# Performance work log

Hardware: AMD Instinct MI355X
Metric: run time of the kernel (lower is better)

The kernel has to match this reference:

```python
import jax, jax.numpy as jnp
import numpy as np

S, B, E, D, A = 4096, 16, 1024, 1024, 512


def setup_inputs() -> dict:
    key = jax.random.key(0)
    ks = jax.random.split(key, 8)
    inv = lambda n: 1.0 / np.sqrt(n)
    return {
        "encoder_padded_last_layer_states": jax.random.normal(ks[0], (S, B, E), jnp.float32),
        "decoder_previous_time_step_state": jax.random.normal(ks[1], (1, B, D), jnp.float32),
        "We": jax.random.uniform(ks[2], (E, A), jnp.float32, -inv(E), inv(E)),
        "be": jax.random.uniform(ks[3], (A,), jnp.float32, -inv(E), inv(E)),
        "Wd": jax.random.uniform(ks[4], (D, A), jnp.float32, -inv(D), inv(D)),
        "bd": jax.random.uniform(ks[5], (A,), jnp.float32, -inv(D), inv(D)),
        "Ws": jax.random.uniform(ks[6], (A, 1), jnp.float32, -inv(A), inv(A)),
        "bs": jax.random.uniform(ks[7], (1,), jnp.float32, -inv(A), inv(A)),
    }


def reference(encoder_padded_last_layer_states, decoder_previous_time_step_state,
              We, be, Wd, bd, Ws, bs):
    enc = encoder_padded_last_layer_states  # [S, B, E]
    dec = decoder_previous_time_step_state  # [1, B, D]
    weighted_e = enc @ We + be              # [S, B, A]
    weighted_d = dec @ Wd + bd              # [1, B, A] broadcasts over S
    scores = jnp.tanh(weighted_e + weighted_d) @ Ws + bs  # [S, B, 1]
    alpha = jax.nn.softmax(scores, axis=0)  # softmax over time dim
    # alpha^T [B,1,S] bmm enc^T [B,S,E] -> [B,1,E] -> squeeze -> [B,E]
    contexts = jnp.einsum("sbo,sbe->be", alpha, enc)
    return contexts
```

## Files before the change

### kernel.cpp

```cpp
#include <hip/hip_runtime.h>
#include <hip/hip_bf16.h>

#define S_DIM 4096
#define B_DIM 16
#define E_DIM 1024
#define D_DIM 1024
#define A_DIM 512
#define M_DIM (S_DIM * B_DIM)

typedef __bf16 bf16x8 __attribute__((ext_vector_type(8)));
typedef float f32x4 __attribute__((ext_vector_type(4)));
typedef unsigned short u16;

__device__ __forceinline__ u16 f2bf(float f) {
    unsigned u = __builtin_bit_cast(unsigned, f);
    u += 0x7fffu + ((u >> 16) & 1u);
    return (u16)(u >> 16);
}

__global__ void k_transpose_we(const float* __restrict__ We, u16* __restrict__ WeT) {
    __shared__ float tile[32][33];
    const int e0 = blockIdx.x * 32;
    const int a0 = blockIdx.y * 32;
    const int tx = threadIdx.x, ty = threadIdx.y;
#pragma unroll
    for (int i = 0; i < 32; i += 8)
        tile[ty + i][tx] = We[(size_t)(e0 + ty + i) * A_DIM + a0 + tx];
    __syncthreads();
#pragma unroll
    for (int i = 0; i < 32; i += 8)
        WeT[(size_t)(a0 + ty + i) * E_DIM + e0 + tx] = f2bf(tile[tx][ty + i]);
}

__global__ void k_comb(const float* __restrict__ dec, const float* __restrict__ Wd,
                       const float* __restrict__ bd, const float* __restrict__ be,
                       float* __restrict__ comb) {
    const int a = blockIdx.x * 256 + threadIdx.x;
    const int b = blockIdx.y;
    float acc = bd[a] + be[a];
    const float* dptr = dec + (size_t)b * D_DIM;
    for (int d = 0; d < D_DIM; ++d)
        acc += dptr[d] * Wd[(size_t)d * A_DIM + a];
    comb[b * A_DIM + a] = acc;
}

__global__ __launch_bounds__(512, 4)
void k_scores(const float* __restrict__ enc, const u16* __restrict__ WeT,
              const float* __restrict__ comb, const float* __restrict__ Wsv,
              const float* __restrict__ bs, float* __restrict__ scores) {
    __shared__ u16 As[64 * 40];
    __shared__ u16 Bs[512 * 40];
    __shared__ float sred[64];

    const int tid  = threadIdx.x;
    const int lane = tid & 63;
    const int wave = tid >> 6;
    const int wr = wave >> 2;
    const int wc = wave & 3;
    const int l15 = lane & 15, lhi = lane >> 4;
    const int blockRow = blockIdx.x * 64;

    if (tid < 64) sred[tid] = 0.f;

    f32x4 acc[2][8];
#pragma unroll
    for (int mf = 0; mf < 2; ++mf)
#pragma unroll
        for (int nf = 0; nf < 8; ++nf)
            acc[mf][nf] = f32x4{0.f, 0.f, 0.f, 0.f};

    const int arow = tid >> 3, ach = tid & 7;
    const int brow = tid >> 2, bch = tid & 3;

    for (int k0 = 0; k0 < E_DIM; k0 += 32) {
        {
            const float4 v = *reinterpret_cast<const float4*>(
                enc + (size_t)(blockRow + arow) * E_DIM + k0 + ach * 4);
            ushort4 h;
            h.x = f2bf(v.x); h.y = f2bf(v.y); h.z = f2bf(v.z); h.w = f2bf(v.w);
            *reinterpret_cast<ushort4*>(&As[arow * 40 + ach * 4]) = h;
        }
#pragma unroll
        for (int p = 0; p < 4; ++p) {
            const int a = brow + p * 128;
            const uint4 w = *reinterpret_cast<const uint4*>(
                WeT + (size_t)a * E_DIM + k0 + bch * 8);
            *reinterpret_cast<uint4*>(&Bs[a * 40 + bch * 8]) = w;
        }
        __syncthreads();

        bf16x8 af[2];
#pragma unroll
        for (int mf = 0; mf < 2; ++mf)
            af[mf] = *reinterpret_cast<const bf16x8*>(
                &As[(wr * 32 + mf * 16 + l15) * 40 + lhi * 8]);
#pragma unroll
        for (int nf = 0; nf < 8; ++nf) {
            const bf16x8 bfv = *reinterpret_cast<const bf16x8*>(
                &Bs[(wc * 128 + nf * 16 + l15) * 40 + lhi * 8]);
            acc[0][nf] = __builtin_amdgcn_mfma_f32_16x16x32_bf16(af[0], bfv, acc[0][nf], 0, 0, 0);
            acc[1][nf] = __builtin_amdgcn_mfma_f32_16x16x32_bf16(af[1], bfv, acc[1][nf], 0, 0, 0);
        }
        __syncthreads();
    }

    float part[2][4] = {{0, 0, 0, 0}, {0, 0, 0, 0}};
#pragma unroll
    for (int nf = 0; nf < 8; ++nf) {
        const int C = wc * 128 + nf * 16 + l15;
        const float wsv = Wsv[C];
#pragma unroll
        for (int mf = 0; mf < 2; ++mf) {
#pragma unroll
            for (int j = 0; j < 4; ++j) {
                const int Rl = wr * 32 + mf * 16 + lhi * 4 + j;
                const int b = (blockRow + Rl) & (B_DIM - 1);
                const float x = acc[mf][nf][j] + comb[b * A_DIM + C];
                const float e = __expf(-2.f * fabsf(x));
                float th = (1.f - e) / (1.f + e);
                th = (x < 0.f) ? -th : th;
                part[mf][j] += th * wsv;
            }
        }
    }
#pragma unroll
    for (int off = 1; off < 16; off <<= 1)
#pragma unroll
        for (int mf = 0; mf < 2; ++mf)
#pragma unroll
            for (int j = 0; j < 4; ++j)
                part[mf][j] += __shfl_xor(part[mf][j], off, 64);
    if (l15 == 0) {
#pragma unroll
        for (int mf = 0; mf < 2; ++mf)
#pragma unroll
            for (int j = 0; j < 4; ++j)
                atomicAdd(&sred[wr * 32 + mf * 16 + lhi * 4 + j], part[mf][j]);
    }
    __syncthreads();
    if (tid < 64) {
        const int r = blockRow + tid;
        scores[(size_t)(r & (B_DIM - 1)) * S_DIM + (r >> 4)] = sred[tid] + bs[0];
    }
}

__global__ void k_softmax(const float* __restrict__ scores, float* __restrict__ alpha) {
    __shared__ float red[8];
    const int b = blockIdx.x;
    const int tid = threadIdx.x;
    const float* sc = scores + (size_t)b * S_DIM;
    float m = -1e30f;
    for (int i = tid; i < S_DIM; i += 256) m = fmaxf(m, sc[i]);
#pragma unroll
    for (int off = 32; off; off >>= 1) m = fmaxf(m, __shfl_xor(m, off, 64));
    if ((tid & 63) == 0) red[tid >> 6] = m;
    __syncthreads();
    m = fmaxf(fmaxf(red[0], red[1]), fmaxf(red[2], red[3]));
    float s = 0.f;
    for (int i = tid; i < S_DIM; i += 256) s += __expf(sc[i] - m);
#pragma unroll
    for (int off = 32; off; off >>= 1) s += __shfl_xor(s, off, 64);
    if ((tid & 63) == 0) red[4 + (tid >> 6)] = s;
    __syncthreads();
    const float inv = 1.f / (red[4] + red[5] + red[6] + red[7]);
    float* al = alpha + (size_t)b * S_DIM;
    for (int i = tid; i < S_DIM; i += 256) al[i] = __expf(sc[i] - m) * inv;
}

__global__ void k_context(const float* __restrict__ enc, const float* __restrict__ alpha,
                          float* __restrict__ out) {
    const int b = blockIdx.y;
    const int chunk = blockIdx.x;
    const int tid = threadIdx.x;
    const int s0 = chunk * 64;
    float4 accv = make_float4(0.f, 0.f, 0.f, 0.f);
    for (int s = 0; s < 64; ++s) {
        const float al = alpha[(size_t)b * S_DIM + s0 + s];
        const float4 v = *reinterpret_cast<const float4*>(
            enc + ((size_t)(s0 + s) * B_DIM + b) * E_DIM + tid * 4);
        accv.x += al * v.x; accv.y += al * v.y;
        accv.z += al * v.z; accv.w += al * v.w;
    }
    float* o = out + (size_t)b * E_DIM + tid * 4;
    atomicAdd(o + 0, accv.x);
    atomicAdd(o + 1, accv.y);
    atomicAdd(o + 2, accv.z);
    atomicAdd(o + 3, accv.w);
}

extern "C" void kernel_launch(void* const* d_in, const int* in_sizes, int n_in,
                              void* d_out, int out_size, void* d_ws, size_t ws_size,
                              hipStream_t stream) {
    const float* enc = (const float*)d_in[0];
    const float* dec = (const float*)d_in[1];
    const float* We  = (const float*)d_in[2];
    const float* be  = (const float*)d_in[3];
    const float* Wd  = (const float*)d_in[4];
    const float* bd  = (const float*)d_in[5];
    const float* Ws  = (const float*)d_in[6];
    const float* bs  = (const float*)d_in[7];
    float* out = (float*)d_out;

    char* ws = (char*)d_ws;
    u16*   WeT    = (u16*)ws;
    float* comb   = (float*)(ws + (1 << 20));
    float* scores = (float*)(ws + (1 << 20) + (32 << 10));
    float* alpha  = (float*)(ws + (1 << 20) + (32 << 10) + (256 << 10));

    hipLaunchKernelGGL(k_transpose_we, dim3(E_DIM / 32, A_DIM / 32), dim3(32, 8), 0, stream,
                       We, WeT);
    hipLaunchKernelGGL(k_comb, dim3(A_DIM / 256, B_DIM), dim3(256), 0, stream,
                       dec, Wd, bd, be, comb);
    hipLaunchKernelGGL(k_scores, dim3(M_DIM / 64), dim3(512), 0, stream,
                       enc, WeT, comb, Ws, bs, scores);
    hipLaunchKernelGGL(k_softmax, dim3(B_DIM), dim3(256), 0, stream, scores, alpha);
    hipMemsetAsync(d_out, 0, (size_t)B_DIM * E_DIM * sizeof(float), stream);
    hipLaunchKernelGGL(k_context, dim3(S_DIM / 64, B_DIM), dim3(256), 0, stream,
                       enc, alpha, out);
}
```

Baseline: 543.6 us.

## Rework score GEMM with swizzled pre-tiled weights, direct LDS loads, and deterministic context reduction

Weights are pre-converted to bf16 in per-K-slab tiles with an XOR swizzle, so the score GEMM can stream them straight into LDS via global_load_lds. The GEMM block drops to 256 threads with 4x8 MFMA tiles per wave and K slabs of 64, and the combined bias is cached in LDS for the tanh epilogue. The decoder projection is split across four waves and reduced in shared memory. The bs bias is dropped because softmax ignores a constant shift. The context atomics and memset are replaced by a two-pass partial-sum reduction. The risks are lower occupancy and larger LDS use per block.

New measurement: 490.5 us. 1.11x faster.

```diff
diff --git a/kernel.cpp b/kernel.cpp
--- a/kernel.cpp
+++ b/kernel.cpp
@@ -7,6 +7,9 @@
 #define D_DIM 1024
 #define A_DIM 512
 #define M_DIM (S_DIM * B_DIM)
+#define BK 64
+#define NKS (E_DIM / BK)
+#define MT 64
 
 typedef __bf16 bf16x8 __attribute__((ext_vector_type(8)));
 typedef float f32x4 __attribute__((ext_vector_type(4)));
@@ -17,105 +20,139 @@
     u += 0x7fffu + ((u >> 16) & 1u);
     return (u16)(u >> 16);
 }
-
-__global__ void k_transpose_we(const float* __restrict__ We, u16* __restrict__ WeT) {
-    __shared__ float tile[32][33];
-    const int e0 = blockIdx.x * 32;
-    const int a0 = blockIdx.y * 32;
-    const int tx = threadIdx.x, ty = threadIdx.y;
-#pragma unroll
-    for (int i = 0; i < 32; i += 8)
-        tile[ty + i][tx] = We[(size_t)(e0 + ty + i) * A_DIM + a0 + tx];
-    __syncthreads();
-#pragma unroll
-    for (int i = 0; i < 32; i += 8)
-        WeT[(size_t)(a0 + ty + i) * E_DIM + e0 + tx] = f2bf(tile[tx][ty + i]);
+__device__ __forceinline__ unsigned pack2(float a, float b) {
+    return (unsigned)f2bf(a) | ((unsigned)f2bf(b) << 16);
+}
+
+__device__ __forceinline__ void gload_lds16(const void* g, void* l) {
+    __builtin_amdgcn_global_load_lds(
+        (const __attribute__((address_space(1))) unsigned*)g,
+        (__attribute__((address_space(3))) unsigned*)l, 16, 0, 0);
+}
+
+__global__ void k_prep_we(const float* __restrict__ We, u16* __restrict__ WeT) {
+    const int gid = blockIdx.x * 256 + threadIdx.x;
+    const int ks = gid >> 12, rem = gid & 4095;
+    const int a = rem >> 3, d = rem & 7;
+    const int c = d ^ (a & 7);
+    const int e0 = ks * BK + c * 8;
+    float v[8];
+#pragma unroll
+    for (int i = 0; i < 8; ++i) v[i] = We[(size_t)(e0 + i) * A_DIM + a];
+    uint4 h;
+    h.x = pack2(v[0], v[1]); h.y = pack2(v[2], v[3]);
+    h.z = pack2(v[4], v[5]); h.w = pack2(v[6], v[7]);
+    *reinterpret_cast<uint4*>(WeT + (size_t)ks * A_DIM * BK + a * BK + d * 8) = h;
 }
 
 __global__ void k_comb(const float* __restrict__ dec, const float* __restrict__ Wd,
                        const float* __restrict__ bd, const float* __restrict__ be,
                        float* __restrict__ comb) {
-    const int a = blockIdx.x * 256 + threadIdx.x;
+    __shared__ float red[4][64];
+    const int a0 = blockIdx.x * 64;
     const int b = blockIdx.y;
-    float acc = bd[a] + be[a];
-    const float* dptr = dec + (size_t)b * D_DIM;
-    for (int d = 0; d < D_DIM; ++d)
-        acc += dptr[d] * Wd[(size_t)d * A_DIM + a];
-    comb[b * A_DIM + a] = acc;
-}
-
-__global__ __launch_bounds__(512, 4)
+    const int t = threadIdx.x;
+    const int al = t & 63, w = t >> 6;
+    float acc = 0.f;
+    const float* dp = dec + (size_t)b * D_DIM + w * 256;
+    const float* wp = Wd + (size_t)w * 256 * A_DIM + a0 + al;
+    for (int d = 0; d < 256; ++d)
+        acc += dp[d] * wp[(size_t)d * A_DIM];
+    red[w][al] = acc;
+    __syncthreads();
+    if (t < 64)
+        comb[b * A_DIM + a0 + t] =
+            red[0][t] + red[1][t] + red[2][t] + red[3][t] + bd[a0 + t] + be[a0 + t];
+}
+
+__global__ __launch_bounds__(256, 2)
 void k_scores(const float* __restrict__ enc, const u16* __restrict__ WeT,
               const float* __restrict__ comb, const float* __restrict__ Wsv,
-              const float* __restrict__ bs, float* __restrict__ scores) {
-    __shared__ u16 As[64 * 40];
-    __shared__ u16 Bs[512 * 40];
-    __shared__ float sred[64];
-
-    const int tid  = threadIdx.x;
+              float* __restrict__ scores) {
+    __shared__ __align__(16) u16 As[MT * BK];
+    __shared__ __align__(16) u16 Bs[A_DIM * BK];
+
+    const int tid = threadIdx.x;
     const int lane = tid & 63;
-    const int wave = tid >> 6;
-    const int wr = wave >> 2;
-    const int wc = wave & 3;
+    const int wc = tid >> 6;
     const int l15 = lane & 15, lhi = lane >> 4;
-    const int blockRow = blockIdx.x * 64;
-
-    if (tid < 64) sred[tid] = 0.f;
-
-    f32x4 acc[2][8];
-#pragma unroll
-    for (int mf = 0; mf < 2; ++mf)
+    const int blockRow = blockIdx.x * MT;
+
+    f32x4 acc[4][8];
+#pragma unroll
+    for (int mf = 0; mf < 4; ++mf)
 #pragma unroll
         for (int nf = 0; nf < 8; ++nf)
             acc[mf][nf] = f32x4{0.f, 0.f, 0.f, 0.f};
 
-    const int arow = tid >> 3, ach = tid & 7;
-    const int brow = tid >> 2, bch = tid & 3;
-
-    for (int k0 = 0; k0 < E_DIM; k0 += 32) {
-        {
-            const float4 v = *reinterpret_cast<const float4*>(
-                enc + (size_t)(blockRow + arow) * E_DIM + k0 + ach * 4);
-            ushort4 h;
-            h.x = f2bf(v.x); h.y = f2bf(v.y); h.z = f2bf(v.z); h.w = f2bf(v.w);
-            *reinterpret_cast<ushort4*>(&As[arow * 40 + ach * 4]) = h;
-        }
-#pragma unroll
-        for (int p = 0; p < 4; ++p) {
-            const int a = brow + p * 128;
-            const uint4 w = *reinterpret_cast<const uint4*>(
-                WeT + (size_t)a * E_DIM + k0 + bch * 8);
-            *reinterpret_cast<uint4*>(&Bs[a * 40 + bch * 8]) = w;
+    const int bOff = wc * 16384 + lane * 16;
+
+    for (int ks = 0; ks < NKS; ++ks) {
+        const int k0 = ks * BK;
+        const char* gsrc = (const char*)WeT + (size_t)ks * A_DIM * BK * 2 + bOff;
+        char* ldst = (char*)Bs + bOff;
+#pragma unroll
+        for (int i = 0; i < 16; ++i)
+            gload_lds16(gsrc + i * 1024, ldst + i * 1024);
+#pragma unroll
+        for (int h = 0; h < 2; ++h) {
+            const int g = tid + h * 256;
+            const int r = g >> 3, d = g & 7;
+            const int c = d ^ (r & 7);
+            const float* src = enc + (size_t)(blockRow + r) * E_DIM + k0 + c * 8;
+            const float4 v0 = *reinterpret_cast<const float4*>(src);
+            const float4 v1 = *reinterpret_cast<const float4*>(src + 4);
+            uint4 hh;
+            hh.x = pack2(v0.x, v0.y); hh.y = pack2(v0.z, v0.w);
+            hh.z = pack2(v1.x, v1.y); hh.w = pack2(v1.z, v1.w);
+            *reinterpret_cast<uint4*>((char*)As + r * 128 + d * 16) = hh;
         }
         __syncthreads();
-
-        bf16x8 af[2];
-#pragma unroll
-        for (int mf = 0; mf < 2; ++mf)
-            af[mf] = *reinterpret_cast<const bf16x8*>(
-                &As[(wr * 32 + mf * 16 + l15) * 40 + lhi * 8]);
-#pragma unroll
-        for (int nf = 0; nf < 8; ++nf) {
-            const bf16x8 bfv = *reinterpret_cast<const bf16x8*>(
-                &Bs[(wc * 128 + nf * 16 + l15) * 40 + lhi * 8]);
-            acc[0][nf] = __builtin_amdgcn_mfma_f32_16x16x32_bf16(af[0], bfv, acc[0][nf], 0, 0, 0);
-            acc[1][nf] = __builtin_amdgcn_mfma_f32_16x16x32_bf16(af[1], bfv, acc[1][nf], 0, 0, 0);
+#pragma unroll
+        for (int kk = 0; kk < 2; ++kk) {
+            bf16x8 af[4];
+#pragma unroll
+            for (int mf = 0; mf < 4; ++mf) {
+                const int rr = mf * 16 + l15;
+                af[mf] = *reinterpret_cast<const bf16x8*>(
+                    (const char*)As + rr * 128 + ((kk * 64 + lhi * 16) ^ ((rr & 7) << 4)));
+            }
+#pragma unroll
+            for (int nf = 0; nf < 8; ++nf) {
+                const int br = wc * 128 + nf * 16 + l15;
+                const bf16x8 bfv = *reinterpret_cast<const bf16x8*>(
+                    (const char*)Bs + br * 128 + ((kk * 64 + lhi * 16) ^ ((br & 7) << 4)));
+#pragma unroll
+                for (int mf = 0; mf < 4; ++mf)
+                    acc[mf][nf] = __builtin_amdgcn_mfma_f32_16x16x32_bf16(
+                        af[mf], bfv, acc[mf][nf], 0, 0, 0);
+            }
         }
         __syncthreads();
     }
 
-    float part[2][4] = {{0, 0, 0, 0}, {0, 0, 0, 0}};
+    float* combLDS = reinterpret_cast<float*>(Bs);
+    float* sred = reinterpret_cast<float*>(As);
+#pragma unroll
+    for (int i = 0; i < 8; ++i) {
+        const int idx = tid + i * 256;
+        reinterpret_cast<float4*>(combLDS)[idx] = reinterpret_cast<const float4*>(comb)[idx];
+    }
+    if (tid < MT) sred[tid] = 0.f;
+    __syncthreads();
+
+    float part[4][4] = {};
 #pragma unroll
     for (int nf = 0; nf < 8; ++nf) {
         const int C = wc * 128 + nf * 16 + l15;
         const float wsv = Wsv[C];
 #pragma unroll
-        for (int mf = 0; mf < 2; ++mf) {
+        for (int mf = 0; mf < 4; ++mf) {
 #pragma unroll
             for (int j = 0; j < 4; ++j) {
-                const int Rl = wr * 32 + mf * 16 + lhi * 4 + j;
+                const int Rl = mf * 16 + lhi * 4 + j;
                 const int b = (blockRow + Rl) & (B_DIM - 1);
-                const float x = acc[mf][nf][j] + comb[b * A_DIM + C];
+                const float x = acc[mf][nf][j] + combLDS[b * A_DIM + C];
                 const float e = __expf(-2.f * fabsf(x));
                 float th = (1.f - e) / (1.f + e);
                 th = (x < 0.f) ? -th : th;
@@ -126,21 +163,21 @@
 #pragma unroll
     for (int off = 1; off < 16; off <<= 1)
 #pragma unroll
-        for (int mf = 0; mf < 2; ++mf)
+        for (int mf = 0; mf < 4; ++mf)
 #pragma unroll
             for (int j = 0; j < 4; ++j)
                 part[mf][j] += __shfl_xor(part[mf][j], off, 64);
     if (l15 == 0) {
 #pragma unroll
-        for (int mf = 0; mf < 2; ++mf)
+        for (int mf = 0; mf < 4; ++mf)
 #pragma unroll
             for (int j = 0; j < 4; ++j)
-                atomicAdd(&sred[wr * 32 + mf * 16 + lhi * 4 + j], part[mf][j]);
-    }
-    __syncthreads();
-    if (tid < 64) {
-        const int r = blockRow + tid;
-        scores[(size_t)(r & (B_DIM - 1)) * S_DIM + (r >> 4)] = sred[tid] + bs[0];
+                atomicAdd(&sred[mf * 16 + lhi * 4 + j], part[mf][j]);
+    }
+    __syncthreads();
+    if (tid < MT) {
+        const int rr = blockRow + tid;
+        scores[(size_t)(rr & (B_DIM - 1)) * S_DIM + (rr >> 4)] = sred[tid];
     }
 }
 
@@ -167,25 +204,29 @@
     for (int i = tid; i < S_DIM; i += 256) al[i] = __expf(sc[i] - m) * inv;
 }
 
-__global__ void k_context(const float* __restrict__ enc, const float* __restrict__ alpha,
-                          float* __restrict__ out) {
-    const int b = blockIdx.y;
-    const int chunk = blockIdx.x;
-    const int tid = threadIdx.x;
-    const int s0 = chunk * 64;
-    float4 accv = make_float4(0.f, 0.f, 0.f, 0.f);
+__global__ void k_ctx1(const float* __restrict__ enc, const float* __restrict__ alpha,
+                       float* __restrict__ partial) {
+    const int b = blockIdx.y, ch = blockIdx.x, tid = threadIdx.x;
+    const int s0 = ch * 64;
+    float4 av = make_float4(0.f, 0.f, 0.f, 0.f);
+    const float* al = alpha + (size_t)b * S_DIM + s0;
     for (int s = 0; s < 64; ++s) {
-        const float al = alpha[(size_t)b * S_DIM + s0 + s];
+        const float a = al[s];
         const float4 v = *reinterpret_cast<const float4*>(
             enc + ((size_t)(s0 + s) * B_DIM + b) * E_DIM + tid * 4);
-        accv.x += al * v.x; accv.y += al * v.y;
-        accv.z += al * v.z; accv.w += al * v.w;
-    }
-    float* o = out + (size_t)b * E_DIM + tid * 4;
-    atomicAdd(o + 0, accv.x);
-    atomicAdd(o + 1, accv.y);
-    atomicAdd(o + 2, accv.z);
-    atomicAdd(o + 3, accv.w);
+        av.x += a * v.x; av.y += a * v.y; av.z += a * v.z; av.w += a * v.w;
+    }
+    reinterpret_cast<float4*>(partial)[((size_t)b * 64 + ch) * 256 + tid] = av;
+}
+
+__global__ void k_ctx2(const float* __restrict__ partial, float* __restrict__ out) {
+    const int b = blockIdx.x, tid = threadIdx.x;
+    float4 s = make_float4(0.f, 0.f, 0.f, 0.f);
+    for (int c = 0; c < 64; ++c) {
+        const float4 v = reinterpret_cast<const float4*>(partial)[((size_t)b * 64 + c) * 256 + tid];
+        s.x += v.x; s.y += v.y; s.z += v.z; s.w += v.w;
+    }
+    reinterpret_cast<float4*>(out)[b * 256 + tid] = s;
 }
 
 extern "C" void kernel_launch(void* const* d_in, const int* in_sizes, int n_in,
@@ -198,23 +239,22 @@
     const float* Wd  = (const float*)d_in[4];
     const float* bd  = (const float*)d_in[5];
     const float* Ws  = (const float*)d_in[6];
-    const float* bs  = (const float*)d_in[7];
     float* out = (float*)d_out;
 
     char* ws = (char*)d_ws;
-    u16*   WeT    = (u16*)ws;
-    float* comb   = (float*)(ws + (1 << 20));
-    float* scores = (float*)(ws + (1 << 20) + (32 << 10));
-    float* alpha  = (float*)(ws + (1 << 20) + (32 << 10) + (256 << 10));
-
-    hipLaunchKernelGGL(k_transpose_we, dim3(E_DIM / 32, A_DIM / 32), dim3(32, 8), 0, stream,
-                       We, WeT);
-    hipLaunchKernelGGL(k_comb, dim3(A_DIM / 256, B_DIM), dim3(256), 0, stream,
+    u16*   WeT     = (u16*)ws;
+    float* comb    = (float*)(ws + (1 << 20));
+    float* scores  = (float*)(ws + (1 << 20) + (32 << 10));
+    float* alpha   = (float*)(ws + (1 << 20) + (288 << 10));
+    float* partial = (float*)(ws + (1 << 20) + (544 << 10));
+
+    hipLaunchKernelGGL(k_prep_we, dim3(256), dim3(256), 0, stream, We, WeT);
+    hipLaunchKernelGGL(k_comb, dim3(A_DIM / 64, B_DIM), dim3(256), 0, stream,
                        dec, Wd, bd, be, comb);
-    hipLaunchKernelGGL(k_scores, dim3(M_DIM / 64), dim3(512), 0, stream,
-                       enc, WeT, comb, Ws, bs, scores);
+    hipLaunchKernelGGL(k_scores, dim3(M_DIM / MT), dim3(256), 0, stream,
+                       enc, WeT, comb, Ws, scores);
     hipLaunchKernelGGL(k_softmax, dim3(B_DIM), dim3(256), 0, stream, scores, alpha);
-    hipMemsetAsync(d_out, 0, (size_t)B_DIM * E_DIM * sizeof(float), stream);
-    hipLaunchKernelGGL(k_context, dim3(S_DIM / 64, B_DIM), dim3(256), 0, stream,
-                       enc, alpha, out);
-}
+    hipLaunchKernelGGL(k_ctx1, dim3(S_DIM / 64, B_DIM), dim3(256), 0, stream,
+                       enc, alpha, partial);
+    hipLaunchKernelGGL(k_ctx2, dim3(B_DIM), dim3(256), 0, stream, partial, out);
+}
```
